# Performance work log

Measured on AMD Instinct MI355X. Metric: run time of the kernel, lower is better.

Reference implementation:

```python
import jax, jax.numpy as jnp
import numpy as np

NM, ND, E, H, HEADS = 1043, 2166, 512, 512, 8
EMM, EDD = 66752, 138624


def setup_inputs() -> dict:
    ks = iter(jax.random.split(jax.random.key(0), 64))
    def nk():
        return next(ks)
    s = 0.05
    inp = {
        'mirna_x': jax.random.normal(nk(), (NM, E), jnp.float32),
        'drug_x': jax.random.normal(nk(), (ND, E), jnp.float32),
    }
    for name, n, m in [('mm1', NM, EMM), ('mm2', NM, EMM), ('dd1', ND, EDD), ('dd2', ND, EDD)]:
        inp['edge_' + name] = jax.random.randint(nk(), (2, m), 0, n, jnp.int32)
        inp['attr_' + name] = jax.random.uniform(nk(), (m,), jnp.float32)
    for enc in ['m1', 'm2', 'd1', 'd2']:
        inp[enc + '_W1'] = jax.random.normal(nk(), (E, H), jnp.float32) * s
        inp[enc + '_b1'] = jax.random.normal(nk(), (H,), jnp.float32) * s
        inp[enc + '_W2'] = jax.random.normal(nk(), (H, H), jnp.float32) * s
        inp[enc + '_b2'] = jax.random.normal(nk(), (H,), jnp.float32) * s
    for p in ['mir', 'drug']:
        for w in ['Wq', 'Wk', 'Wv', 'Wo']:
            inp[p + '_' + w] = jax.random.normal(nk(), (E, E), jnp.float32) * s
        inp[p + '_fw'] = jax.random.normal(nk(), (4,), jnp.float32) * 0.5
        inp[p + '_fb'] = jax.random.normal(nk(), (1,), jnp.float32) * s
    return inp


def gcn_conv(x, W, b, edge, w):
    # PyG GCNConv: add self-loops (weight 1), symmetric normalization, aggregate at target.
    n = x.shape[0]
    h = x @ W
    loop = jnp.arange(n, dtype=edge.dtype)
    src = jnp.concatenate([edge[0], loop])
    dst = jnp.concatenate([edge[1], loop])
    ww = jnp.concatenate([w, jnp.ones((n,), w.dtype)])
    deg = jax.ops.segment_sum(ww, dst, num_segments=n)
    dis = jnp.where(deg > 0, jax.lax.rsqrt(deg), 0.0)
    norm = dis[src] * ww * dis[dst]  # [E+n]
    out = jax.ops.segment_sum(norm[:, None] * h[src], dst, num_segments=n)
    return out + b


def gcn_encoder(x, edge, w, W1, b1, W2, b2):
    x1 = jax.nn.relu(gcn_conv(x, W1, b1, edge, w))
    x2 = jax.nn.relu(gcn_conv(x1, W2, b2, edge, w))
    return jnp.concatenate([x1, x2], axis=1)  # [N, 2H]


def mha(x, Wq, Wk, Wv, Wo):
    # x: (views=4, N, E); attention over the N (num_features) axis, per view.
    V, N, _ = x.shape
    hd = E // HEADS
    def split(W):
        return (x @ W).reshape(V, N, HEADS, hd).transpose(0, 2, 1, 3)  # (V, h, N, hd)
    q, k, v = split(Wq), split(Wk), split(Wv)
    scores = jnp.einsum('vhnd,vhmd->vhnm', q, k) / jnp.sqrt(jnp.float32(hd))
    a = jax.nn.softmax(scores, axis=-1)
    o = jnp.einsum('vhnm,vhmd->vhnd', a, v).transpose(0, 2, 1, 3).reshape(V, N, E)
    return o @ Wo


def fuse(o, fw, fb):
    # 1x1 Conv2d over 4 channels -> weighted channel sum + bias, then view(E,-1).t()
    y = jnp.einsum('c,cne->ne', fw, o) + fb  # (N, E)
    return y.reshape(E, -1).T  # torch .view(out_channels, -1).t() on row-major data


def view_pipeline(v1, v2, Wq, Wk, Wv, Wo, fw, fb):
    emb = jnp.concatenate([v1, v2], axis=1)  # (N, 4E)
    N = emb.shape[0]
    # torch: .view(1, 4, E, -1) then transpose_(-1, -2) -> (4, N, E) after dropping batch dim
    x = emb.reshape(4, E, N).transpose(0, 2, 1)
    return fuse(mha(x, Wq, Wk, Wv, Wo), fw, fb)


def reference(mirna_x, drug_x, edge_mm1, attr_mm1, edge_mm2, attr_mm2, edge_dd1, attr_dd1, edge_dd2, attr_dd2, m1_W1, m1_b1, m1_W2, m1_b2, m2_W1, m2_b1, m2_W2, m2_b2, d1_W1, d1_b1, d1_W2, d1_b2, d2_W1, d2_b1, d2_W2, d2_b2, mir_Wq, mir_Wk, mir_Wv, mir_Wo, mir_fw, mir_fb, drug_Wq, drug_Wk, drug_Wv, drug_Wo, drug_fw, drug_fb):
    mv1 = gcn_encoder(mirna_x, edge_mm1, attr_mm1, m1_W1, m1_b1, m1_W2, m1_b2)
    mv2 = gcn_encoder(mirna_x, edge_mm2, attr_mm2, m2_W1, m2_b1, m2_W2, m2_b2)
    dv1 = gcn_encoder(drug_x, edge_dd1, attr_dd1, d1_W1, d1_b1, d1_W2, d1_b2)
    dv2 = gcn_encoder(drug_x, edge_dd2, attr_dd2, d2_W1, d2_b1, d2_W2, d2_b2)
    mir = view_pipeline(mv1, mv2, mir_Wq, mir_Wk, mir_Wv, mir_Wo, mir_fw, mir_fb)
    drg = view_pipeline(dv1, dv2, drug_Wq, drug_Wk, drug_Wv, drug_Wo, drug_fw, drug_fb)
    return mir @ drg.T  # (1043, 2166)
```

## Files before the change

### kernel.cpp

```cpp
#include <hip/hip_runtime.h>
#include <cmath>

#define NM 1043
#define ND 2166

static inline int ceil_div(int a, int b) { return (a + b - 1) / b; }

typedef __attribute__((ext_vector_type(8))) short bf16x8;
typedef __attribute__((ext_vector_type(4))) float f32x4;
typedef __attribute__((ext_vector_type(2))) unsigned int u32x2;
typedef __attribute__((ext_vector_type(4))) unsigned int u32x4;

union U8 { u32x4 u; bf16x8 h; };

__device__ inline unsigned int pkbf(float a, float b) {
  unsigned int ua = __float_as_uint(a), ub = __float_as_uint(b);
  ua += 0x7FFFu + ((ua >> 16) & 1);
  ub += 0x7FFFu + ((ub >> 16) & 1);
  return (ub & 0xFFFF0000u) | (ua >> 16);
}

__device__ inline unsigned short bf1(float a) {
  unsigned int ua = __float_as_uint(a);
  ua += 0x7FFFu + ((ua >> 16) & 1);
  return (unsigned short)(ua >> 16);
}

struct PrepW { const float* W[16]; unsigned short* Wt[16]; };

__global__ __launch_bounds__(256) void prep_w(PrepW p) {
  const int z = blockIdx.z;
  const float* __restrict__ W = p.W[z];
  unsigned short* __restrict__ Wt = p.Wt[z];
  const int n0 = blockIdx.x * 64, k0 = blockIdx.y * 64;
  __shared__ float Ws[64][65];
  const int tid = threadIdx.x;
#pragma unroll
  for (int it = 0; it < 16; it++) {
    int i = it * 256 + tid;
    int k = i >> 6, n = i & 63;
    Ws[k][n] = W[(size_t)(k0 + k) * 512 + n0 + n];
  }
  __syncthreads();
#pragma unroll
  for (int it = 0; it < 16; it++) {
    int i = it * 256 + tid;
    int n = i >> 6, k = i & 63;
    Wt[(size_t)(n0 + n) * 512 + k0 + k] = bf1(Ws[k][n]);
  }
}

struct BGemm {
  const void* A[6]; const unsigned short* Bt[6]; void* C[6];
  int M[6]; int lda[6];
};

template<int AIN_BF16, int COUT_BF16>
__global__ __launch_bounds__(256) void gemm_mfma(BGemm g) {
  const int z = blockIdx.z;
  const int M = g.M[z];
  const int bm = blockIdx.y << 7;
  if (bm >= M) return;
  const int bn = blockIdx.x << 7;
  const int lda = g.lda[z];
  const char* __restrict__ Ab = (const char*)g.A[z];
  const char* __restrict__ Btb = (const char*)g.Bt[z];

  __shared__ short As_s[128 * 64];
  __shared__ short Bs_s[128 * 64];
  char* asb = (char*)As_s;
  char* bsb = (char*)Bs_s;

  const int tid = threadIdx.x;
  const int lane = tid & 63;
  const int w = tid >> 6;
  const int wm = (w >> 1) << 6, wn = (w & 1) << 6;
  const int fr = lane & 15, kg = lane >> 4;

  f32x4 acc[4][4];
#pragma unroll
  for (int i = 0; i < 4; i++)
#pragma unroll
    for (int j = 0; j < 4; j++) acc[i][j] = (f32x4){0.f, 0.f, 0.f, 0.f};

  for (int kb = 0; kb < 512; kb += 64) {
    __syncthreads();
#pragma unroll
    for (int qi = 0; qi < 4; qi++) {
      int qid = qi * 256 + tid;
      int mm = qid >> 3, qk = qid & 7;
      u32x4 wv = {0u, 0u, 0u, 0u};
      if (bm + mm < M) {
        if (AIN_BF16) {
          wv = *(const u32x4*)(Ab + ((size_t)(bm + mm) * lda + kb + qk * 8) * 2);
        } else {
          const float* ap = (const float*)Ab + (size_t)(bm + mm) * lda + kb + qk * 8;
          float4 f0 = ((const float4*)ap)[0];
          float4 f1 = ((const float4*)ap)[1];
          wv.x = pkbf(f0.x, f0.y); wv.y = pkbf(f0.z, f0.w);
          wv.z = pkbf(f1.x, f1.y); wv.w = pkbf(f1.z, f1.w);
        }
      }
      *(u32x4*)(asb + mm * 128 + ((qk * 16) ^ ((mm & 7) << 4))) = wv;
    }
#pragma unroll
    for (int qi = 0; qi < 4; qi++) {
      int qid = qi * 256 + tid;
      int nn = qid >> 3, qk = qid & 7;
      u32x4 bv = *(const u32x4*)(Btb + (((size_t)(bn + nn)) << 10) + (kb + qk * 8) * 2);
      *(u32x4*)(bsb + nn * 128 + ((qk * 16) ^ ((nn & 7) << 4))) = bv;
    }
    __syncthreads();

#pragma unroll
    for (int ks = 0; ks < 2; ks++) {
      bf16x8 af[4], bfv[4];
#pragma unroll
      for (int i = 0; i < 4; i++) {
        int row = wm + i * 16 + fr;
        af[i] = *(const bf16x8*)(asb + row * 128 + (((ks * 64) + kg * 16) ^ ((row & 7) << 4)));
      }
#pragma unroll
      for (int j = 0; j < 4; j++) {
        int row = wn + j * 16 + fr;
        bfv[j] = *(const bf16x8*)(bsb + row * 128 + (((ks * 64) + kg * 16) ^ ((row & 7) << 4)));
      }
#pragma unroll
      for (int i = 0; i < 4; i++)
#pragma unroll
        for (int j = 0; j < 4; j++)
          acc[i][j] = __builtin_amdgcn_mfma_f32_16x16x32_bf16(af[i], bfv[j], acc[i][j], 0, 0, 0);
    }
  }

#pragma unroll
  for (int i = 0; i < 4; i++) {
    int m0 = bm + wm + i * 16 + kg * 4;
#pragma unroll
    for (int j = 0; j < 4; j++) {
      int n = bn + wn + j * 16 + fr;
#pragma unroll
      for (int r = 0; r < 4; r++) {
        if (m0 + r < M) {
          if (COUT_BF16) ((unsigned short*)g.C[z])[(size_t)(m0 + r) * 512 + n] = bf1(acc[i][j][r]);
          else ((float*)g.C[z])[(size_t)(m0 + r) * 512 + n] = acc[i][j][r];
        }
      }
    }
  }
}

__global__ __launch_bounds__(256) void gemm_tn(
    const float* __restrict__ A, const float* __restrict__ B, float* __restrict__ C,
    int M, int N, int K, int lda, int ldb, int ldc) {
  __shared__ float As[16][65];
  __shared__ float Bs[16][65];
  const int tid = threadIdx.x;
  const int tx = tid & 15, ty = tid >> 4;
  const int bm = blockIdx.y << 6, bn = blockIdx.x << 6;
  float acc[4][4] = {};
  for (int k0 = 0; k0 < K; k0 += 16) {
    for (int i = tid; i < 16 * 64; i += 256) {
      int kk = i >> 6, mm = i & 63;
      int r = k0 + kk, c = bm + mm;
      As[kk][mm] = (r < K && c < M) ? A[(size_t)r * lda + c] : 0.f;
    }
    for (int i = tid; i < 16 * 64; i += 256) {
      int kk = i >> 6, nn = i & 63;
      int r = k0 + kk, c = bn + nn;
      Bs[kk][nn] = (r < K && c < N) ? B[(size_t)r * ldb + c] : 0.f;
    }
    __syncthreads();
#pragma unroll
    for (int kk = 0; kk < 16; kk++) {
      float a[4], b[4];
#pragma unroll
      for (int i = 0; i < 4; i++) a[i] = As[kk][ty + (i << 4)];
#pragma unroll
      for (int j = 0; j < 4; j++) b[j] = Bs[kk][tx + (j << 4)];
#pragma unroll
      for (int i = 0; i < 4; i++)
#pragma unroll
        for (int j = 0; j < 4; j++) acc[i][j] += a[i] * b[j];
    }
    __syncthreads();
  }
#pragma unroll
  for (int i = 0; i < 4; i++) {
    int r = bm + ty + (i << 4);
    if (r >= M) continue;
#pragma unroll
    for (int j = 0; j < 4; j++) {
      int c = bn + tx + (j << 4);
      if (c < N) C[(size_t)r * ldc + c] = acc[i][j];
    }
  }
}

struct DegB {
  const int* dst[4]; const float* attr[4];
  float* dis[4]; int* cnt[4];
  int epref[5];
};

__global__ __launch_bounds__(256) void deg_count_b(DegB g) {
  int et = blockIdx.x * 256 + threadIdx.x;
  if (et >= g.epref[4]) return;
  int z = (et >= g.epref[1]) + (et >= g.epref[2]) + (et >= g.epref[3]);
  int e = et - g.epref[z];
  int d = g.dst[z][e];
  atomicAdd(&g.dis[z][d], g.attr[z][e]);
  atomicAdd(&g.cnt[z][d], 1);
}

struct FinB { float* dis[4]; int n[4]; };

__global__ __launch_bounds__(256) void finish_dis_b(FinB g) {
  int z = blockIdx.z;
  int i = blockIdx.x * 256 + threadIdx.x;
  if (i < g.n[z]) g.dis[z][i] = rsqrtf(g.dis[z][i] + 1.0f);
}

struct ScanB { const int* cnt[4]; int* rowptr[4]; int n[4]; };

__global__ __launch_bounds__(256) void scan_b(ScanB s) {
  int z = blockIdx.x;
  int n = s.n[z];
  const int* cnt = s.cnt[z];
  int* rp = s.rowptr[z];
  __shared__ int sums[256];
  int tid = threadIdx.x;
  int chunk = (n + 255) >> 8;
  int start = tid * chunk;
  int local = 0;
  for (int i = 0; i < chunk; i++) {
    int idx = start + i;
    if (idx < n) local += cnt[idx];
  }
  sums[tid] = local;
  __syncthreads();
  for (int off = 1; off < 256; off <<= 1) {
    int t = (tid >= off) ? sums[tid - off] : 0;
    __syncthreads();
    sums[tid] += t;
    __syncthreads();
  }
  int base = sums[tid] - local;
  int total = sums[255];
  int run = base;
  for (int i = 0; i < chunk; i++) {
    int idx = start + i;
    if (idx < n) { rp[idx] = run; run += cnt[idx]; }
  }
  if (tid == 0) rp[n] = total;
}

struct FillB {
  const int* src[4]; const int* dst[4]; const float* attr[4];
  const int* rowptr[4]; int* cur[4]; int* col[4]; float* val[4];
  int epref[5];
};

__global__ __launch_bounds__(256) void fill_b(FillB f) {
  int et = blockIdx.x * 256 + threadIdx.x;
  if (et >= f.epref[4]) return;
  int z = (et >= f.epref[1]) + (et >= f.epref[2]) + (et >= f.epref[3]);
  int e = et - f.epref[z];
  int d = f.dst[z][e];
  int pos = f.rowptr[z][d] + atomicAdd(&f.cur[z][d], 1);
  f.col[z][pos] = f.src[z][e];
  f.val[z][pos] = f.attr[z][e];
}

struct GathB {
  const int* rowptr[4]; const int* col[4]; const float* val[4];
  const float* dis[4]; const float* h[4]; const float* b[4];
  float* out[4]; int n[4];
};

__global__ __launch_bounds__(256) void gcn_gather_b(GathB c) {
  const int z = blockIdx.z;
  const int node = blockIdx.x;
  if (node >= c.n[z]) return;
  const int tid = threadIdx.x;
  const int* __restrict__ col = c.col[z];
  const float* __restrict__ val = c.val[z];
  const float* __restrict__ dis = c.dis[z];
  const float* __restrict__ h = c.h[z];
  const int beg = c.rowptr[z][node], end = c.rowptr[z][node + 1];
  float acc0 = 0.f, acc1 = 0.f;
  int e = beg;
  for (; e + 4 <= end; e += 4) {
    int s0 = col[e], s1 = col[e + 1], s2 = col[e + 2], s3 = col[e + 3];
    float w0 = val[e] * dis[s0];
    float w1 = val[e + 1] * dis[s1];
    float w2 = val[e + 2] * dis[s2];
    float w3 = val[e + 3] * dis[s3];
    const float* p0 = h + ((size_t)s0 << 9);
    const float* p1 = h + ((size_t)s1 << 9);
    const float* p2 = h + ((size_t)s2 << 9);
    const float* p3 = h + ((size_t)s3 << 9);
    acc0 += w0 * p0[tid] + w1 * p1[tid] + w2 * p2[tid] + w3 * p3[tid];
    acc1 += w0 * p0[tid + 256] + w1 * p1[tid + 256] + w2 * p2[tid + 256] + w3 * p3[tid + 256];
  }
  for (; e < end; e++) {
    int s = col[e];
    float w = val[e] * dis[s];
    const float* p = h + ((size_t)s << 9);
    acc0 += w * p[tid];
    acc1 += w * p[tid + 256];
  }
  const float dd = dis[node];
  const float* hp = h + ((size_t)node << 9);
  float o0 = fmaxf(dd * acc0 + dd * dd * hp[tid] + c.b[z][tid], 0.f);
  float o1 = fmaxf(dd * acc1 + dd * dd * hp[tid + 256] + c.b[z][tid + 256], 0.f);
  float* op = c.out[z] + (size_t)node * 2048;
  op[tid] = o0;
  op[tid + 256] = o1;
}

struct GatherB { const float* emb[2]; float* xv[2]; int n[2]; };

__global__ __launch_bounds__(256) void gather_b(GatherB g) {
  int z = blockIdx.z;
  int n = g.n[z];
  size_t i = (size_t)blockIdx.x * 256 + threadIdx.x;
  if (i >= (size_t)n * 2048) return;
  int e = (int)(i & 511);
  size_t t = i >> 9;
  int v = (int)(t / n);
  int nn = (int)(t - (size_t)v * n);
  g.xv[z][i] = g.emb[z][((size_t)v * 512 + e) * n + nn];
}

struct AttArgs {
  const unsigned short* Q[2]; const unsigned short* K[2]; const unsigned short* V[2];
  unsigned short* O[2]; int N[2];
};

__global__ __launch_bounds__(256) void attn4_kernel(AttArgs ar) {
  const int z = blockIdx.z;
  const int N = ar.N[z];
  const int qb = blockIdx.x * 128;
  if (qb >= N) return;
  const int vh = blockIdx.y, v = vh >> 3, h = vh & 7;
  const size_t base = (size_t)v * N * 512 + (size_t)h * 64;
  const unsigned short* __restrict__ Qb = ar.Q[z] + base;
  const char* __restrict__ Kc = (const char*)(ar.K[z] + base);
  const char* __restrict__ Vc = (const char*)(ar.V[z] + base);
  unsigned short* __restrict__ Ob = ar.O[z] + base;

  __shared__ short kt_s[64 * 64];
  __shared__ short vt_s[64 * 64];
  char* ktb = (char*)kt_s;
  char* vtb = (char*)vt_s;

  const int tid = threadIdx.x;
  const int lane = tid & 63;
  const int w = tid >> 6;
  const int a15 = lane & 15;
  const int g = lane >> 4;

  const int qA = qb + w * 32 + a15;
  const int qB = qA + 16;
  bf16x8 qfA0 = {}, qfA1 = {}, qfB0 = {}, qfB1 = {};
  if (qA < N) {
    qfA0 = *(const bf16x8*)(Qb + (size_t)qA * 512 + g * 8);
    qfA1 = *(const bf16x8*)(Qb + (size_t)qA * 512 + 32 + g * 8);
  }
  if (qB < N) {
    qfB0 = *(const bf16x8*)(Qb + (size_t)qB * 512 + g * 8);
    qfB1 = *(const bf16x8*)(Qb + (size_t)qB * 512 + 32 + g * 8);
  }

  float rmA = -INFINITY, rsA = 0.f, rmB = -INFINITY, rsB = 0.f;
  f32x4 oA0 = {0.f, 0.f, 0.f, 0.f}, oA1 = oA0, oA2 = oA0, oA3 = oA0;
  f32x4 oB0 = oA0, oB1 = oA0, oB2 = oA0, oB3 = oA0;

  const int swzk = (a15 & 7) << 4;
  const int swzv = a15 << 3;
  const int skr = tid >> 2, skq = (tid & 3) * 16;
  const int vsr = tid & 15, vsc = tid >> 4;

  for (int kb = 0; kb < N; kb += 64) {
    __syncthreads();
    {
      const int sw = (skr & 7) << 4;
      const char* kp = Kc + (size_t)(kb + skr) * 1024;
      u32x4 k0 = {0u,0u,0u,0u}, k1 = {0u,0u,0u,0u};
      if (kb + skr < N) {
        k0 = *(const u32x4*)(kp + skq);
        k1 = *(const u32x4*)(kp + skq + 64);
      }
      *(u32x4*)(ktb + skr * 128 + (skq ^ sw)) = k0;
      *(u32x4*)(ktb + skr * 128 + ((skq + 64) ^ sw)) = k1;
    }
    {
      const int r0 = kb + 4 * vsr;
      u32x2 i0 = {0u,0u}, i1 = {0u,0u}, i2 = {0u,0u}, i3 = {0u,0u};
      const char* vp = Vc + (size_t)r0 * 1024 + vsc * 8;
      if (r0 + 0 < N) i0 = *(const u32x2*)(vp);
      if (r0 + 1 < N) i1 = *(const u32x2*)(vp + 1024);
      if (r0 + 2 < N) i2 = *(const u32x2*)(vp + 2048);
      if (r0 + 3 < N) i3 = *(const u32x2*)(vp + 3072);
      const int dd = 4 * vsc, kby = 8 * vsr;
      u32x2 o;
      o.x = (i0.x & 0xFFFFu) | (i1.x << 16); o.y = (i2.x & 0xFFFFu) | (i3.x << 16);
      *(u32x2*)(vtb + (dd + 0) * 128 + (kby ^ (((dd + 0) & 15) << 3))) = o;
      o.x = (i0.x >> 16) | (i1.x & 0xFFFF0000u); o.y = (i2.x >> 16) | (i3.x & 0xFFFF0000u);
      *(u32x2*)(vtb + (dd + 1) * 128 + (kby ^ (((dd + 1) & 15) << 3))) = o;
      o.x = (i0.y & 0xFFFFu) | (i1.y << 16); o.y = (i2.y & 0xFFFFu) | (i3.y << 16);
      *(u32x2*)(vtb + (dd + 2) * 128 + (kby ^ (((dd + 2) & 15) << 3))) = o;
      o.x = (i0.y >> 16) | (i1.y & 0xFFFF0000u); o.y = (i2.y >> 16) | (i3.y & 0xFFFF0000u);
      *(u32x2*)(vtb + (dd + 3) * 128 + (kby ^ (((dd + 3) & 15) << 3))) = o;
    }
    __syncthreads();

    f32x4 sA0 = {0.f,0.f,0.f,0.f}, sA1 = sA0, sA2 = sA0, sA3 = sA0;
    f32x4 sB0 = sA0, sB1 = sA0, sB2 = sA0, sB3 = sA0;
#define QK2(m, sAm, sBm, s2, qfa, qfb) { \
    bf16x8 kf = *(const bf16x8*)(ktb + (16 * m + a15) * 128 + ((64 * s2 + 16 * g) ^ swzk)); \
    sAm = __builtin_amdgcn_mfma_f32_16x16x32_bf16(kf, qfa, sAm, 0, 0, 0); \
    sBm = __builtin_amdgcn_mfma_f32_16x16x32_bf16(kf, qfb, sBm, 0, 0, 0); }
    QK2(0, sA0, sB0, 0, qfA0, qfB0) QK2(1, sA1, sB1, 0, qfA0, qfB0)
    QK2(2, sA2, sB2, 0, qfA0, qfB0) QK2(3, sA3, sB3, 0, qfA0, qfB0)
    QK2(0, sA0, sB0, 1, qfA1, qfB1) QK2(1, sA1, sB1, 1, qfA1, qfB1)
    QK2(2, sA2, sB2, 1, qfA1, qfB1) QK2(3, sA3, sB3, 1, qfA1, qfB1)
#undef QK2

    sA0 *= 0.125f; sA1 *= 0.125f; sA2 *= 0.125f; sA3 *= 0.125f;
    sB0 *= 0.125f; sB1 *= 0.125f; sB2 *= 0.125f; sB3 *= 0.125f;

    if (kb + 64 > N) {
#define MSK(sfm, sgm, m) { int kk = kb + 16 * m + 4 * g; \
      if (kk + 0 >= N) { sfm.x = -INFINITY; sgm.x = -INFINITY; } \
      if (kk + 1 >= N) { sfm.y = -INFINITY; sgm.y = -INFINITY; } \
      if (kk + 2 >= N) { sfm.z = -INFINITY; sgm.z = -INFINITY; } \
      if (kk + 3 >= N) { sfm.w = -INFINITY; sgm.w = -INFINITY; } }
      MSK(sA0, sB0, 0) MSK(sA1, sB1, 1) MSK(sA2, sB2, 2) MSK(sA3, sB3, 3)
#undef MSK
    }

#define SOFTMAX_PV(sf0, sf1, sf2, sf3, rm, rs, q0, q1, q2, q3) { \
    float tmax = fmaxf(fmaxf(fmaxf(sf0.x, sf0.y), fmaxf(sf0.z, sf0.w)), \
                       fmaxf(fmaxf(sf1.x, sf1.y), fmaxf(sf1.z, sf1.w))); \
    tmax = fmaxf(tmax, fmaxf(fmaxf(fmaxf(sf2.x, sf2.y), fmaxf(sf2.z, sf2.w)), \
                             fmaxf(fmaxf(sf3.x, sf3.y), fmaxf(sf3.z, sf3.w)))); \
    tmax = fmaxf(tmax, __shfl_xor(tmax, 16)); \
    tmax = fmaxf(tmax, __shfl_xor(tmax, 32)); \
    const float nm = fmaxf(rm, tmax); \
    const float sc = __expf(rm - nm); \
    float ps = 0.f; \
    u32x4 pr0, pr1, pr2, pr3; \
    SMX(sf0, pr0) SMX(sf1, pr1) SMX(sf2, pr2) SMX(sf3, pr3) \
    ps += __shfl_xor(ps, 16); \
    ps += __shfl_xor(ps, 32); \
    rs = rs * sc + ps; \
    rm = nm; \
    q0 *= sc; q1 *= sc; q2 *= sc; q3 *= sc; \
    U8 pb0, pb1; \
    pb0.u.x = (pr0.x >> 16) | pr0.y;  pb0.u.y = (pr0.z >> 16) | pr0.w; \
    pb0.u.z = (pr1.x >> 16) | pr1.y;  pb0.u.w = (pr1.z >> 16) | pr1.w; \
    pb1.u.x = (pr2.x >> 16) | pr2.y;  pb1.u.y = (pr2.z >> 16) | pr2.w; \
    pb1.u.z = (pr3.x >> 16) | pr3.y;  pb1.u.w = (pr3.z >> 16) | pr3.w; \
    PV(0, q0, 0, pb0.h) PV(1, q1, 0, pb0.h) PV(2, q2, 0, pb0.h) PV(3, q3, 0, pb0.h) \
    PV(0, q0, 1, pb1.h) PV(1, q1, 1, pb1.h) PV(2, q2, 1, pb1.h) PV(3, q3, 1, pb1.h) }

#define SMX(sfm, prm) { float e; unsigned int u; \
    e = __expf(sfm.x - nm); u = __float_as_uint(e); u += 0x7FFFu + ((u >> 16) & 1); u &= 0xFFFF0000u; ps += __uint_as_float(u); prm.x = u; \
    e = __expf(sfm.y - nm); u = __float_as_uint(e); u += 0x7FFFu + ((u >> 16) & 1); u &= 0xFFFF0000u; ps += __uint_as_float(u); prm.y = u; \
    e = __expf(sfm.z - nm); u = __float_as_uint(e); u += 0x7FFFu + ((u >> 16) & 1); u &= 0xFFFF0000u; ps += __uint_as_float(u); prm.z = u; \
    e = __expf(sfm.w - nm); u = __float_as_uint(e); u += 0x7FFFu + ((u >> 16) & 1); u &= 0xFFFF0000u; ps += __uint_as_float(u); prm.w = u; }
#define PV(md, om, s2, pbr) { \
    const char* vr = vtb + (16 * md + a15) * 128; \
    u32x2 v0 = *(const u32x2*)(vr + ((64 * s2 + 8 * g) ^ swzv)); \
    u32x2 v1 = *(const u32x2*)(vr + ((64 * s2 + 32 + 8 * g) ^ swzv)); \
    U8 av; av.u.x = v0.x; av.u.y = v0.y; av.u.z = v1.x; av.u.w = v1.y; \
    om = __builtin_amdgcn_mfma_f32_16x16x32_bf16(av.h, pbr, om, 0, 0, 0); }

    SOFTMAX_PV(sA0, sA1, sA2, sA3, rmA, rsA, oA0, oA1, oA2, oA3)
    SOFTMAX_PV(sB0, sB1, sB2, sB3, rmB, rsB, oB0, oB1, oB2, oB3)
#undef PV
#undef SMX
#undef SOFTMAX_PV
  }

  if (qA < N) {
    const float inv = 1.0f / rsA;
    char* op = (char*)(Ob + (size_t)qA * 512) + g * 8;
    u32x2 r;
    r.x = pkbf(oA0.x * inv, oA0.y * inv); r.y = pkbf(oA0.z * inv, oA0.w * inv);
    *(u32x2*)(op) = r;
    r.x = pkbf(oA1.x * inv, oA1.y * inv); r.y = pkbf(oA1.z * inv, oA1.w * inv);
    *(u32x2*)(op + 32) = r;
    r.x = pkbf(oA2.x * inv, oA2.y * inv); r.y = pkbf(oA2.z * inv, oA2.w * inv);
    *(u32x2*)(op + 64) = r;
    r.x = pkbf(oA3.x * inv, oA3.y * inv); r.y = pkbf(oA3.z * inv, oA3.w * inv);
    *(u32x2*)(op + 96) = r;
  }
  if (qB < N) {
    const float inv = 1.0f / rsB;
    char* op = (char*)(Ob + (size_t)qB * 512) + g * 8;
    u32x2 r;
    r.x = pkbf(oB0.x * inv, oB0.y * inv); r.y = pkbf(oB0.z * inv, oB0.w * inv);
    *(u32x2*)(op) = r;
    r.x = pkbf(oB1.x * inv, oB1.y * inv); r.y = pkbf(oB1.z * inv, oB1.w * inv);
    *(u32x2*)(op + 32) = r;
    r.x = pkbf(oB2.x * inv, oB2.y * inv); r.y = pkbf(oB2.z * inv, oB2.w * inv);
    *(u32x2*)(op + 64) = r;
    r.x = pkbf(oB3.x * inv, oB3.y * inv); r.y = pkbf(oB3.z * inv, oB3.w * inv);
    *(u32x2*)(op + 96) = r;
  }
}

struct FuseB { const float* mha[2]; const float* fw[2]; const float* fb[2]; float* y[2]; int n[2]; };

__global__ __launch_bounds__(256) void fuse_b(FuseB fz) {
  int z = blockIdx.z;
  int n = fz.n[z];
  int i = blockIdx.x * 256 + threadIdx.x;
  if (i >= n * 512) return;
  size_t stride = (size_t)n * 512;
  const float* m = fz.mha[z];
  const float* fw = fz.fw[z];
  float acc = fz.fb[z][0];
  acc += fw[0] * m[i];
  acc += fw[1] * m[stride + i];
  acc += fw[2] * m[2 * stride + i];
  acc += fw[3] * m[3 * stride + i];
  fz.y[z][i] = acc;
}

extern "C" void kernel_launch(void* const* d_in, const int* in_sizes, int n_in,
                              void* d_out, int out_size, void* d_ws, size_t ws_size,
                              hipStream_t stream) {
  const float* mirna_x = (const float*)d_in[0];
  const float* drug_x  = (const float*)d_in[1];
  const int* edge[4] = { (const int*)d_in[2], (const int*)d_in[4], (const int*)d_in[6], (const int*)d_in[8] };
  const float* attr[4] = { (const float*)d_in[3], (const float*)d_in[5], (const float*)d_in[7], (const float*)d_in[9] };
  const int m[4] = { in_sizes[2] / 2, in_sizes[4] / 2, in_sizes[6] / 2, in_sizes[8] / 2 };
  const int nn4[4] = { NM, NM, ND, ND };
  float* out = (float*)d_out;

  float* ws = (float*)d_ws;
  size_t off = 0;
  auto take = [&](size_t nelem) {
    float* r = ws + off;
    off += (nelem + 255) & ~(size_t)255;
    return r;
  };
  const size_t HN = (size_t)NM * 512, HD = (size_t)ND * 512;
  const size_t HALL = 2 * HN + 2 * HD;
  float* emb_m = take((size_t)NM * 2048);
  float* emb_d = take((size_t)ND * 2048);
  float* region = take(2 * HALL);
  float* h4[4] = { region, region + HN, region + 2 * HN, region + 2 * HN + HD };
  float* xv_m = region;
  float* xv_d = region + (size_t)NM * 2048;
  float* dis_all = take(4 * 2560);
  float* dis4[4] = { dis_all, dis_all + 2560, dis_all + 2 * 2560, dis_all + 3 * 2560 };
  int* cnt_all = (int*)take(4 * 2560);
  int* cnt4[4] = { cnt_all, cnt_all + 2560, cnt_all + 2 * 2560, cnt_all + 3 * 2560 };
  int* rp_all = (int*)take(4 * 2304);
  int* rp4[4] = { rp_all, rp_all + 2304, rp_all + 2 * 2304, rp_all + 3 * 2304 };
  int* col4[4];
  float* val4[4];
  for (int z = 0; z < 4; z++) {
    col4[z] = (int*)take(m[z]);
    val4[z] = take(m[z]);
  }
  unsigned short* Qm = (unsigned short*)take((size_t)NM * 2048);
  unsigned short* Km = (unsigned short*)take((size_t)NM * 2048);
  unsigned short* Vm = (unsigned short*)take((size_t)NM * 2048);
  unsigned short* Qd = (unsigned short*)take((size_t)ND * 2048);
  unsigned short* Kd = (unsigned short*)take((size_t)ND * 2048);
  unsigned short* Vd = (unsigned short*)take((size_t)ND * 2048);
  float* mha_m = take((size_t)NM * 2048);
  float* mha_d = take((size_t)ND * 2048);
  float* y_m = take(HN);
  float* y_d = take(HD);
  unsigned short* wt = (unsigned short*)take((size_t)16 * 131072);

  int pref = 0;
  int epref[5];
  for (int z = 0; z < 4; z++) { epref[z] = pref; pref += m[z]; }
  epref[4] = pref;

  PrepW pw;
  for (int z = 0; z < 4; z++) {
    pw.W[z] = (const float*)d_in[10 + 4 * z];
    pw.W[4 + z] = (const float*)d_in[12 + 4 * z];
    pw.W[8 + z] = (const float*)d_in[26 + z];
    pw.W[12 + z] = (const float*)d_in[32 + z];
  }
  for (int z = 0; z < 16; z++) pw.Wt[z] = wt + (size_t)z * 262144;
  prep_w<<<dim3(8, 8, 16), 256, 0, stream>>>(pw);

  hipMemsetAsync(dis_all, 0, 4 * 2560 * sizeof(float), stream);
  hipMemsetAsync(cnt_all, 0, 4 * 2560 * sizeof(int), stream);

  DegB db;
  for (int z = 0; z < 4; z++) {
    db.dst[z] = edge[z] + m[z]; db.attr[z] = attr[z];
    db.dis[z] = dis4[z]; db.cnt[z] = cnt4[z];
  }
  for (int z = 0; z < 5; z++) db.epref[z] = epref[z];
  deg_count_b<<<ceil_div(pref, 256), 256, 0, stream>>>(db);

  FinB fn;
  for (int z = 0; z < 4; z++) { fn.dis[z] = dis4[z]; fn.n[z] = nn4[z]; }
  finish_dis_b<<<dim3(ceil_div(ND, 256), 1, 4), 256, 0, stream>>>(fn);

  ScanB sb;
  for (int z = 0; z < 4; z++) { sb.cnt[z] = cnt4[z]; sb.rowptr[z] = rp4[z]; sb.n[z] = nn4[z]; }
  scan_b<<<4, 256, 0, stream>>>(sb);

  hipMemsetAsync(cnt_all, 0, 4 * 2560 * sizeof(int), stream);
  FillB fl;
  for (int z = 0; z < 4; z++) {
    fl.src[z] = edge[z]; fl.dst[z] = edge[z] + m[z]; fl.attr[z] = attr[z];
    fl.rowptr[z] = rp4[z]; fl.cur[z] = cnt4[z]; fl.col[z] = col4[z]; fl.val[z] = val4[z];
  }
  for (int z = 0; z < 5; z++) fl.epref[z] = epref[z];
  fill_b<<<ceil_div(pref, 256), 256, 0, stream>>>(fl);

  BGemm c1;
  const float* xin[4] = { mirna_x, mirna_x, drug_x, drug_x };
  for (int z = 0; z < 4; z++) {
    c1.A[z] = xin[z]; c1.Bt[z] = wt + (size_t)z * 262144; c1.C[z] = h4[z];
    c1.M[z] = nn4[z]; c1.lda[z] = 512;
  }
  for (int z = 4; z < 6; z++) { c1.A[z] = nullptr; c1.Bt[z] = nullptr; c1.C[z] = nullptr; c1.M[z] = 0; c1.lda[z] = 512; }
  gemm_mfma<0, 0><<<dim3(4, ceil_div(ND, 128), 4), 256, 0, stream>>>(c1);

  float* embp[4] = { emb_m, emb_m + 1024, emb_d, emb_d + 1024 };
  GathB g1;
  for (int z = 0; z < 4; z++) {
    g1.rowptr[z] = rp4[z]; g1.col[z] = col4[z]; g1.val[z] = val4[z];
    g1.dis[z] = dis4[z]; g1.h[z] = h4[z]; g1.b[z] = (const float*)d_in[11 + 4 * z];
    g1.out[z] = embp[z]; g1.n[z] = nn4[z];
  }
  gcn_gather_b<<<dim3(ND, 1, 4), 256, 0, stream>>>(g1);

  BGemm c2 = c1;
  for (int z = 0; z < 4; z++) {
    c2.A[z] = embp[z]; c2.Bt[z] = wt + (size_t)(4 + z) * 262144; c2.C[z] = h4[z];
    c2.M[z] = nn4[z]; c2.lda[z] = 2048;
  }
  gemm_mfma<0, 0><<<dim3(4, ceil_div(ND, 128), 4), 256, 0, stream>>>(c2);

  GathB g2 = g1;
  for (int z = 0; z < 4; z++) { g2.b[z] = (const float*)d_in[13 + 4 * z]; g2.out[z] = embp[z] + 512; }
  gcn_gather_b<<<dim3(ND, 1, 4), 256, 0, stream>>>(g2);

  GatherB gt;
  gt.emb[0] = emb_m; gt.emb[1] = emb_d; gt.xv[0] = xv_m; gt.xv[1] = xv_d;
  gt.n[0] = NM; gt.n[1] = ND;
  gather_b<<<dim3(ceil_div(ND * 2048, 256), 1, 2), 256, 0, stream>>>(gt);

  BGemm qkv;
  unsigned short* qkvc[6] = { Qm, Km, Vm, Qd, Kd, Vd };
  for (int z = 0; z < 6; z++) {
    qkv.A[z] = (z < 3) ? xv_m : xv_d;
    qkv.Bt[z] = wt + (size_t)((z < 3) ? (8 + z) : (12 + z - 3)) * 262144;
    qkv.C[z] = qkvc[z];
    qkv.M[z] = (z < 3) ? 4 * NM : 4 * ND; qkv.lda[z] = 512;
  }
  gemm_mfma<0, 1><<<dim3(4, ceil_div(4 * ND, 128), 6), 256, 0, stream>>>(qkv);

  AttArgs aa;
  aa.Q[0] = Qm; aa.K[0] = Km; aa.V[0] = Vm; aa.O[0] = (unsigned short*)xv_m; aa.N[0] = NM;
  aa.Q[1] = Qd; aa.K[1] = Kd; aa.V[1] = Vd; aa.O[1] = (unsigned short*)xv_d; aa.N[1] = ND;
  attn4_kernel<<<dim3(ceil_div(ND, 128), 32, 2), 256, 0, stream>>>(aa);

  BGemm wo;
  for (int z = 0; z < 2; z++) {
    wo.A[z] = (z == 0) ? xv_m : xv_d;
    wo.Bt[z] = wt + (size_t)(z == 0 ? 11 : 15) * 262144;
    wo.C[z] = (z == 0) ? mha_m : mha_d;
    wo.M[z] = (z == 0) ? 4 * NM : 4 * ND; wo.lda[z] = 512;
  }
  for (int z = 2; z < 6; z++) { wo.A[z] = nullptr; wo.Bt[z] = nullptr; wo.C[z] = nullptr; wo.M[z] = 0; wo.lda[z] = 512; }
  gemm_mfma<1, 0><<<dim3(4, ceil_div(4 * ND, 128), 2), 256, 0, stream>>>(wo);

  FuseB fz;
  fz.mha[0] = mha_m; fz.mha[1] = mha_d;
  fz.fw[0] = (const float*)d_in[30]; fz.fw[1] = (const float*)d_in[36];
  fz.fb[0] = (const float*)d_in[31]; fz.fb[1] = (const float*)d_in[37];
  fz.y[0] = y_m; fz.y[1] = y_d;
  fz.n[0] = NM; fz.n[1] = ND;
  fuse_b<<<dim3(ceil_div(ND * 512, 256), 1, 2), 256, 0, stream>>>(fz);

  gemm_tn<<<dim3(ceil_div(ND, 64), ceil_div(NM, 64)), 256, 0, stream>>>(
      y_m, y_d, out, NM, ND, 512, NM, ND, ND);
}
```

Measured before the change: 830.0 us.

## Split attention key range across two blocks and merge partial softmax results

Attention now splits the key tiles into two halves, one per block, so the grid doubles. Each block writes unnormalized fp32 partial outputs plus running max and sum, and a new merge kernel combines them with log-sum-exp weights and packs to bf16. The softmax also switches to exp2 with the scale folded in as log2(e)/8. This trades extra fp32 global traffic and one more launch for better occupancy on a small grid; the Q/K/V buffer allocations were also halved to match bf16 sizing.

After: 848.5 us. 2.2% more time.

```diff
diff --git a/kernel.cpp b/kernel.cpp
--- a/kernel.cpp
+++ b/kernel.cpp
@@ -3,6 +3,7 @@
 
 #define NM 1043
 #define ND 2166
+#define KS 2
 
 static inline int ceil_div(int a, int b) { return (a + b - 1) / b; }
 
@@ -333,22 +334,29 @@
   g.xv[z][i] = g.emb[z][((size_t)v * 512 + e) * n + nn];
 }
 
+#define ATT_SC 0.18033688011112042f
+
 struct AttArgs {
   const unsigned short* Q[2]; const unsigned short* K[2]; const unsigned short* V[2];
-  unsigned short* O[2]; int N[2];
+  float* Op[2];
+  float* ml[2];
+  int N[2];
 };
 
-__global__ __launch_bounds__(256) void attn4_kernel(AttArgs ar) {
+__global__ __launch_bounds__(256) void attn5_kernel(AttArgs ar) {
   const int z = blockIdx.z;
   const int N = ar.N[z];
-  const int qb = blockIdx.x * 128;
+  const int qi = blockIdx.x / KS, ks = blockIdx.x % KS;
+  const int qb = qi * 128;
   if (qb >= N) return;
   const int vh = blockIdx.y, v = vh >> 3, h = vh & 7;
   const size_t base = (size_t)v * N * 512 + (size_t)h * 64;
   const unsigned short* __restrict__ Qb = ar.Q[z] + base;
   const char* __restrict__ Kc = (const char*)(ar.K[z] + base);
   const char* __restrict__ Vc = (const char*)(ar.V[z] + base);
-  unsigned short* __restrict__ Ob = ar.O[z] + base;
+  const size_t sstride = (size_t)4 * N * 512;
+  float* __restrict__ Opb = ar.Op[z] + (size_t)ks * sstride + base;
+  float* __restrict__ mlb = ar.ml[z] + (size_t)ks * 4 * N * 16;
 
   __shared__ short kt_s[64 * 64];
   __shared__ short vt_s[64 * 64];
@@ -382,7 +390,13 @@
   const int skr = tid >> 2, skq = (tid & 3) * 16;
   const int vsr = tid & 15, vsc = tid >> 4;
 
-  for (int kb = 0; kb < N; kb += 64) {
+  const int nt = (N + 63) >> 6;
+  const int nth = nt >> 1;
+  const int t0 = ks ? nth : 0;
+  const int t1 = ks ? nt : nth;
+
+  for (int t = t0; t < t1; t++) {
+    const int kb = t << 6;
     __syncthreads();
     {
       const int sw = (skr & 7) << 4;
@@ -428,8 +442,8 @@
     QK2(2, sA2, sB2, 1, qfA1, qfB1) QK2(3, sA3, sB3, 1, qfA1, qfB1)
 #undef QK2
 
-    sA0 *= 0.125f; sA1 *= 0.125f; sA2 *= 0.125f; sA3 *= 0.125f;
-    sB0 *= 0.125f; sB1 *= 0.125f; sB2 *= 0.125f; sB3 *= 0.125f;
+    sA0 *= ATT_SC; sA1 *= ATT_SC; sA2 *= ATT_SC; sA3 *= ATT_SC;
+    sB0 *= ATT_SC; sB1 *= ATT_SC; sB2 *= ATT_SC; sB3 *= ATT_SC;
 
     if (kb + 64 > N) {
 #define MSK(sfm, sgm, m) { int kk = kb + 16 * m + 4 * g; \
@@ -441,6 +455,17 @@
 #undef MSK
     }
 
+#define SMX(sfm, prm) { float e; unsigned int u; \
+    e = exp2f(sfm.x - nm); u = __float_as_uint(e); u += 0x7FFFu + ((u >> 16) & 1); u &= 0xFFFF0000u; ps += __uint_as_float(u); prm.x = u; \
+    e = exp2f(sfm.y - nm); u = __float_as_uint(e); u += 0x7FFFu + ((u >> 16) & 1); u &= 0xFFFF0000u; ps += __uint_as_float(u); prm.y = u; \
+    e = exp2f(sfm.z - nm); u = __float_as_uint(e); u += 0x7FFFu + ((u >> 16) & 1); u &= 0xFFFF0000u; ps += __uint_as_float(u); prm.z = u; \
+    e = exp2f(sfm.w - nm); u = __float_as_uint(e); u += 0x7FFFu + ((u >> 16) & 1); u &= 0xFFFF0000u; ps += __uint_as_float(u); prm.w = u; }
+#define PV(md, om, s2, pbr) { \
+    const char* vr = vtb + (16 * md + a15) * 128; \
+    u32x2 v0 = *(const u32x2*)(vr + ((64 * s2 + 8 * g) ^ swzv)); \
+    u32x2 v1 = *(const u32x2*)(vr + ((64 * s2 + 32 + 8 * g) ^ swzv)); \
+    U8 av; av.u.x = v0.x; av.u.y = v0.y; av.u.z = v1.x; av.u.w = v1.y; \
+    om = __builtin_amdgcn_mfma_f32_16x16x32_bf16(av.h, pbr, om, 0, 0, 0); }
 #define SOFTMAX_PV(sf0, sf1, sf2, sf3, rm, rs, q0, q1, q2, q3) { \
     float tmax = fmaxf(fmaxf(fmaxf(sf0.x, sf0.y), fmaxf(sf0.z, sf0.w)), \
                        fmaxf(fmaxf(sf1.x, sf1.y), fmaxf(sf1.z, sf1.w))); \
@@ -449,7 +474,7 @@
     tmax = fmaxf(tmax, __shfl_xor(tmax, 16)); \
     tmax = fmaxf(tmax, __shfl_xor(tmax, 32)); \
     const float nm = fmaxf(rm, tmax); \
-    const float sc = __expf(rm - nm); \
+    const float sc = exp2f(rm - nm); \
     float ps = 0.f; \
     u32x4 pr0, pr1, pr2, pr3; \
     SMX(sf0, pr0) SMX(sf1, pr1) SMX(sf2, pr2) SMX(sf3, pr3) \
@@ -466,51 +491,67 @@
     PV(0, q0, 0, pb0.h) PV(1, q1, 0, pb0.h) PV(2, q2, 0, pb0.h) PV(3, q3, 0, pb0.h) \
     PV(0, q0, 1, pb1.h) PV(1, q1, 1, pb1.h) PV(2, q2, 1, pb1.h) PV(3, q3, 1, pb1.h) }
 
-#define SMX(sfm, prm) { float e; unsigned int u; \
-    e = __expf(sfm.x - nm); u = __float_as_uint(e); u += 0x7FFFu + ((u >> 16) & 1); u &= 0xFFFF0000u; ps += __uint_as_float(u); prm.x = u; \
-    e = __expf(sfm.y - nm); u = __float_as_uint(e); u += 0x7FFFu + ((u >> 16) & 1); u &= 0xFFFF0000u; ps += __uint_as_float(u); prm.y = u; \
-    e = __expf(sfm.z - nm); u = __float_as_uint(e); u += 0x7FFFu + ((u >> 16) & 1); u &= 0xFFFF0000u; ps += __uint_as_float(u); prm.z = u; \
-    e = __expf(sfm.w - nm); u = __float_as_uint(e); u += 0x7FFFu + ((u >> 16) & 1); u &= 0xFFFF0000u; ps += __uint_as_float(u); prm.w = u; }
-#define PV(md, om, s2, pbr) { \
-    const char* vr = vtb + (16 * md + a15) * 128; \
-    u32x2 v0 = *(const u32x2*)(vr + ((64 * s2 + 8 * g) ^ swzv)); \
-    u32x2 v1 = *(const u32x2*)(vr + ((64 * s2 + 32 + 8 * g) ^ swzv)); \
-    U8 av; av.u.x = v0.x; av.u.y = v0.y; av.u.z = v1.x; av.u.w = v1.y; \
-    om = __builtin_amdgcn_mfma_f32_16x16x32_bf16(av.h, pbr, om, 0, 0, 0); }
-
     SOFTMAX_PV(sA0, sA1, sA2, sA3, rmA, rsA, oA0, oA1, oA2, oA3)
     SOFTMAX_PV(sB0, sB1, sB2, sB3, rmB, rsB, oB0, oB1, oB2, oB3)
+#undef SOFTMAX_PV
 #undef PV
 #undef SMX
-#undef SOFTMAX_PV
   }
 
   if (qA < N) {
-    const float inv = 1.0f / rsA;
-    char* op = (char*)(Ob + (size_t)qA * 512) + g * 8;
-    u32x2 r;
-    r.x = pkbf(oA0.x * inv, oA0.y * inv); r.y = pkbf(oA0.z * inv, oA0.w * inv);
-    *(u32x2*)(op) = r;
-    r.x = pkbf(oA1.x * inv, oA1.y * inv); r.y = pkbf(oA1.z * inv, oA1.w * inv);
-    *(u32x2*)(op + 32) = r;
-    r.x = pkbf(oA2.x * inv, oA2.y * inv); r.y = pkbf(oA2.z * inv, oA2.w * inv);
-    *(u32x2*)(op + 64) = r;
-    r.x = pkbf(oA3.x * inv, oA3.y * inv); r.y = pkbf(oA3.z * inv, oA3.w * inv);
-    *(u32x2*)(op + 96) = r;
+    float* op = Opb + (size_t)qA * 512 + 4 * g;
+    *(f32x4*)(op + 0)  = oA0;
+    *(f32x4*)(op + 16) = oA1;
+    *(f32x4*)(op + 32) = oA2;
+    *(f32x4*)(op + 48) = oA3;
+    if (g == 0) {
+      float* mp = mlb + ((size_t)v * N + qA) * 16 + h * 2;
+      mp[0] = rmA; mp[1] = rsA;
+    }
   }
   if (qB < N) {
-    const float inv = 1.0f / rsB;
-    char* op = (char*)(Ob + (size_t)qB * 512) + g * 8;
-    u32x2 r;
-    r.x = pkbf(oB0.x * inv, oB0.y * inv); r.y = pkbf(oB0.z * inv, oB0.w * inv);
-    *(u32x2*)(op) = r;
-    r.x = pkbf(oB1.x * inv, oB1.y * inv); r.y = pkbf(oB1.z * inv, oB1.w * inv);
-    *(u32x2*)(op + 32) = r;
-    r.x = pkbf(oB2.x * inv, oB2.y * inv); r.y = pkbf(oB2.z * inv, oB2.w * inv);
-    *(u32x2*)(op + 64) = r;
-    r.x = pkbf(oB3.x * inv, oB3.y * inv); r.y = pkbf(oB3.z * inv, oB3.w * inv);
-    *(u32x2*)(op + 96) = r;
-  }
+    float* op = Opb + (size_t)qB * 512 + 4 * g;
+    *(f32x4*)(op + 0)  = oB0;
+    *(f32x4*)(op + 16) = oB1;
+    *(f32x4*)(op + 32) = oB2;
+    *(f32x4*)(op + 48) = oB3;
+    if (g == 0) {
+      float* mp = mlb + ((size_t)v * N + qB) * 16 + h * 2;
+      mp[0] = rmB; mp[1] = rsB;
+    }
+  }
+}
+
+struct MergeB {
+  const float* Op[2]; const float* ml[2];
+  unsigned short* O[2]; int N[2];
+};
+
+__global__ __launch_bounds__(256) void attn_merge_b(MergeB mg) {
+  const int z = blockIdx.z;
+  const int N = mg.N[z];
+  const size_t tot = (size_t)4 * N * 128;
+  size_t idx = (size_t)blockIdx.x * 256 + threadIdx.x;
+  if (idx >= tot) return;
+  const size_t i = idx * 4;
+  const size_t nq = i >> 9;
+  const int e = (int)(i & 511);
+  const int h = e >> 6;
+  const size_t sstride = (size_t)4 * N * 512;
+  const float* mlp0 = mg.ml[z] + nq * 16 + h * 2;
+  const float* mlp1 = mg.ml[z] + (size_t)4 * N * 16 + nq * 16 + h * 2;
+  const float m0 = mlp0[0], l0 = mlp0[1];
+  const float m1 = mlp1[0], l1 = mlp1[1];
+  const float mm = fmaxf(m0, m1);
+  const float w0 = exp2f(m0 - mm), w1 = exp2f(m1 - mm);
+  const float inv = 1.0f / (l0 * w0 + l1 * w1);
+  const float4 a = *(const float4*)(mg.Op[z] + i);
+  const float4 b = *(const float4*)(mg.Op[z] + sstride + i);
+  const float s0 = w0 * inv, s1 = w1 * inv;
+  u32x2 r;
+  r.x = pkbf(a.x * s0 + b.x * s1, a.y * s0 + b.y * s1);
+  r.y = pkbf(a.z * s0 + b.z * s1, a.w * s0 + b.w * s1);
+  *(u32x2*)(mg.O[z] + i) = r;
 }
 
 struct FuseB { const float* mha[2]; const float* fw[2]; const float* fb[2]; float* y[2]; int n[2]; };
@@ -569,17 +610,21 @@
     col4[z] = (int*)take(m[z]);
     val4[z] = take(m[z]);
   }
-  unsigned short* Qm = (unsigned short*)take((size_t)NM * 2048);
-  unsigned short* Km = (unsigned short*)take((size_t)NM * 2048);
-  unsigned short* Vm = (unsigned short*)take((size_t)NM * 2048);
-  unsigned short* Qd = (unsigned short*)take((size_t)ND * 2048);
-  unsigned short* Kd = (unsigned short*)take((size_t)ND * 2048);
-  unsigned short* Vd = (unsigned short*)take((size_t)ND * 2048);
+  unsigned short* Qm = (unsigned short*)take((size_t)NM * 1024);
+  unsigned short* Km = (unsigned short*)take((size_t)NM * 1024);
+  unsigned short* Vm = (unsigned short*)take((size_t)NM * 1024);
+  unsigned short* Qd = (unsigned short*)take((size_t)ND * 1024);
+  unsigned short* Kd = (unsigned short*)take((size_t)ND * 1024);
+  unsigned short* Vd = (unsigned short*)take((size_t)ND * 1024);
   float* mha_m = take((size_t)NM * 2048);
   float* mha_d = take((size_t)ND * 2048);
   float* y_m = take(HN);
   float* y_d = take(HD);
   unsigned short* wt = (unsigned short*)take((size_t)16 * 131072);
+  float* Op_m = take((size_t)KS * NM * 2048);
+  float* Op_d = take((size_t)KS * ND * 2048);
+  float* ml_m = take((size_t)KS * NM * 4 * 16);
+  float* ml_d = take((size_t)KS * ND * 4 * 16);
 
   int pref = 0;
   int epref[5];
@@ -669,9 +714,14 @@
   gemm_mfma<0, 1><<<dim3(4, ceil_div(4 * ND, 128), 6), 256, 0, stream>>>(qkv);
 
   AttArgs aa;
-  aa.Q[0] = Qm; aa.K[0] = Km; aa.V[0] = Vm; aa.O[0] = (unsigned short*)xv_m; aa.N[0] = NM;
-  aa.Q[1] = Qd; aa.K[1] = Kd; aa.V[1] = Vd; aa.O[1] = (unsigned short*)xv_d; aa.N[1] = ND;
-  attn4_kernel<<<dim3(ceil_div(ND, 128), 32, 2), 256, 0, stream>>>(aa);
+  aa.Q[0] = Qm; aa.K[0] = Km; aa.V[0] = Vm; aa.Op[0] = Op_m; aa.ml[0] = ml_m; aa.N[0] = NM;
+  aa.Q[1] = Qd; aa.K[1] = Kd; aa.V[1] = Vd; aa.Op[1] = Op_d; aa.ml[1] = ml_d; aa.N[1] = ND;
+  attn5_kernel<<<dim3(ceil_div(ND, 128) * KS, 32, 2), 256, 0, stream>>>(aa);
+
+  MergeB mg;
+  mg.Op[0] = Op_m; mg.ml[0] = ml_m; mg.O[0] = (unsigned short*)xv_m; mg.N[0] = NM;
+  mg.Op[1] = Op_d; mg.ml[1] = ml_d; mg.O[1] = (unsigned short*)xv_d; mg.N[1] = ND;
+  attn_merge_b<<<dim3(ceil_div(4 * ND * 128, 256), 1, 2), 256, 0, stream>>>(mg);
 
   BGemm wo;
   for (int z = 0; z < 2; z++) {
```
